# Kernel tuning notes

Measured on AMD Instinct MI355X. Metric: run time of the kernel, lower is better.

Reference implementation:

```python
import jax, jax.numpy as jnp
import numpy as np

B, N, M = 8, 1024, 1024
DIM2 = 1280          # config.dim * 2
KIN = 1344           # esm_dim + cell_line_dim
H, DK = 8, 64        # heads, attn_dim_key
SCALE = DK ** -0.5


def setup_inputs() -> dict:
    key = jax.random.key(0)
    ks = jax.random.split(key, 7)
    rna_reps = jax.random.normal(ks[0], (B, N, DIM2), dtype=jnp.float32)
    protein_reps = jax.random.normal(ks[1], (B, M, KIN), dtype=jnp.float32)
    # learned params (Linear stores weight [out, in])
    Wq = jax.random.normal(ks[2], (H * DK, DIM2), dtype=jnp.float32) * (DIM2 ** -0.5)
    bq = jnp.zeros((H * DK,), dtype=jnp.float32)
    Wk = jax.random.normal(ks[3], (H * DK, KIN), dtype=jnp.float32) * (KIN ** -0.5)
    bk = jnp.zeros((H * DK,), dtype=jnp.float32)
    rel_bias = jax.random.normal(ks[4], (1, H, 1, DK), dtype=jnp.float32)
    return {"rna_reps": rna_reps, "protein_reps": protein_reps,
            "Wq": Wq, "bq": bq, "Wk": Wk, "bk": bk, "rel_bias": rel_bias}


def reference(rna_reps, protein_reps, Wq, bq, Wk, bk, rel_bias):
    b = rna_reps.shape[0]
    q = rna_reps @ Wq.T + bq           # [b, n, h*dk]
    k = protein_reps @ Wk.T + bk       # [b, m, h*dk]
    q = q.reshape(b, N, H, DK).transpose(0, 2, 1, 3)   # b h n d
    k = k.reshape(b, M, H, DK).transpose(0, 2, 1, 3)   # b h m d
    q = q * SCALE
    logits = jnp.einsum('bhid,bhjd->bhij', q + rel_bias, k)  # [b,h,n,m]
    out = jnp.mean(logits, axis=1)     # mean over heads -> [b,n,m]
    # dropout p=0.0 (eval) -> identity
    return out
```

## Files before the change

### kernel.cpp

```cpp
#include <hip/hip_runtime.h>
#include <hip/hip_bf16.h>


typedef __bf16 bf16x8 __attribute__((ext_vector_type(8)));
typedef __bf16 bf16x4 __attribute__((ext_vector_type(4)));
typedef float f32x4 __attribute__((ext_vector_type(4)));

__device__ inline bf16x4 cvt4(const f32x4 a) {
    bf16x4 r;
    r[0] = (__bf16)a[0]; r[1] = (__bf16)a[1];
    r[2] = (__bf16)a[2]; r[3] = (__bf16)a[3];
    return r;
}

__global__ __launch_bounds__(256, 2)
void proj_all(const float* __restrict__ rna,  const float* __restrict__ prot,
              const float* __restrict__ Wq,   const float* __restrict__ bq,
              const float* __restrict__ Wk,   const float* __restrict__ bk,
              const float* __restrict__ rb,
              __bf16* __restrict__ qout, __bf16* __restrict__ kout)
{
    __shared__ __bf16 AS[2][128 * 64];
    __shared__ __bf16 WS[2][128 * 64];

    const int bid = blockIdx.x;
    const int wg  = (bid & 7) * 64 + (bid >> 3);
    const bool isQ = wg < 256;
    const int lwg  = isQ ? wg : wg - 256;
    const int brow = (lwg >> 2) * 128;
    const int bcol = (lwg & 3) * 128;

    const float* A    = isQ ? rna : prot;
    const float* W    = isQ ? Wq  : Wk;
    const float* bias = isQ ? bq  : bk;
    __bf16*      out  = isQ ? qout : kout;
    const int    K    = isQ ? 1280 : 1344;
    const int    nt   = K >> 6;

    const int tid  = threadIdx.x;
    const int lane = tid & 63;
    const int wid  = tid >> 6;
    const int wr   = wid >> 1;
    const int wc   = wid & 1;
    const int fr   = lane & 15;
    const int q4   = lane >> 4;

    const int rloc = wid * 32 + q4;
    const float* aGlob = A + (size_t)(brow + rloc) * K + fr * 4;
    const float* wGlob = W + (size_t)(bcol + rloc) * K + fr * 4;
    const int lb = rloc * 128 + (((fr >> 1) ^ (q4 << 1)) << 4) + (lane & 1) * 8;

    const int rmask = ((fr & 3) << 1) | ((fr >> 2) & 1);

    f32x4 acc[4][4] = {};
    f32x4 ra[8], rw[8];

    #pragma unroll
    for (int i = 0; i < 8; ++i) {
        ra[i] = *(const f32x4*)(aGlob + (size_t)(i * 4) * K);
        rw[i] = *(const f32x4*)(wGlob + (size_t)(i * 4) * K);
    }

    for (int t = 0; t < nt; ++t) {
        char* as = (char*)AS[t & 1];
        char* ws = (char*)WS[t & 1];
        __syncthreads();
        #pragma unroll
        for (int i = 0; i < 8; ++i) {
            *(bf16x4*)(as + ((lb ^ ((i & 1) << 4)) + i * 512)) = cvt4(ra[i]);
            *(bf16x4*)(ws + ((lb ^ ((i & 1) << 4)) + i * 512)) = cvt4(rw[i]);
        }
        if (t + 1 < nt) {
            const int k0n = (t + 1) * 64;
            #pragma unroll
            for (int i = 0; i < 8; ++i) {
                ra[i] = *(const f32x4*)(aGlob + (size_t)(i * 4) * K + k0n);
                rw[i] = *(const f32x4*)(wGlob + (size_t)(i * 4) * K + k0n);
            }
        }
        __builtin_amdgcn_sched_barrier(0);
        __syncthreads();

        #pragma unroll
        for (int kk = 0; kk < 2; ++kk) {
            bf16x8 af[4], bw[4];
            #pragma unroll
            for (int m = 0; m < 4; ++m)
                af[m] = *(const bf16x8*)(as + (wr * 64 + m * 16 + fr) * 128
                                            + (((kk * 4 + q4) ^ rmask) << 4));
            #pragma unroll
            for (int n = 0; n < 4; ++n)
                bw[n] = *(const bf16x8*)(ws + (wc * 64 + n * 16 + fr) * 128
                                            + (((kk * 4 + q4) ^ rmask) << 4));
            #pragma unroll
            for (int m = 0; m < 4; ++m)
                #pragma unroll
                for (int n = 0; n < 4; ++n)
                    acc[m][n] = __builtin_amdgcn_mfma_f32_16x16x32_bf16(af[m], bw[n], acc[m][n], 0, 0, 0);
        }
    }

    const int r0 = (lane >> 4) * 4;
    #pragma unroll
    for (int n = 0; n < 4; ++n) {
        const int c = bcol + wc * 64 + n * 16 + fr;
        const float bv = bias[c];
        const float rv = isQ ? rb[c] : 0.0f;
        #pragma unroll
        for (int m = 0; m < 4; ++m) {
            const int row = brow + wr * 64 + m * 16 + r0;
            #pragma unroll
            for (int j = 0; j < 4; ++j) {
                float v = acc[m][n][j] + bv;
                if (isQ) v = 0.125f * v + rv;
                out[(size_t)(row + j) * 512 + c] = (__bf16)v;
            }
        }
    }
}

__global__ __launch_bounds__(256, 2)
void attn_kernel(const __bf16* __restrict__ Q,
                 const __bf16* __restrict__ Kb,
                 float* __restrict__ out)
{
    __shared__ __bf16 As[128 * 64];
    __shared__ __bf16 Bs[128 * 64];

    const int tid  = threadIdx.x;
    const int lane = tid & 63;
    const int wid  = tid >> 6;
    const int wr   = wid >> 1;
    const int wc   = wid & 1;
    const int b    = blockIdx.z;
    const int brow = blockIdx.y * 128;
    const int bcol = blockIdx.x * 128;

    const __bf16* Qb = Q  + (size_t)b * 1024 * 512;
    const __bf16* Kp = Kb + (size_t)b * 1024 * 512;

    const int fr = lane & 15;
    const int q4 = lane >> 4;

    f32x4 acc[4][4] = {};

    const int lr3 = lane >> 3;
    const int m3  = ((lr3 & 3) << 1) | ((lr3 >> 2) & 1);
    const int scol = ((lane & 7) ^ m3) * 8;
    const int rmask = ((fr & 3) << 1) | ((fr >> 2) & 1);

    for (int k0 = 0; k0 < 512; k0 += 64) {
        __syncthreads();
        #pragma unroll
        for (int i = 0; i < 4; ++i) {
            const int rbase = wid * 32 + i * 8;
            const __bf16* sa = Qb + (size_t)(brow + rbase + lr3) * 512 + k0 + scol;
            const __bf16* sb = Kp + (size_t)(bcol + rbase + lr3) * 512 + k0 + scol;
            __builtin_amdgcn_global_load_lds(
                (const __attribute__((address_space(1))) void*)sa,
                (__attribute__((address_space(3))) void*)&As[rbase * 64], 16, 0, 0);
            __builtin_amdgcn_global_load_lds(
                (const __attribute__((address_space(1))) void*)sb,
                (__attribute__((address_space(3))) void*)&Bs[rbase * 64], 16, 0, 0);
        }
        __syncthreads();

        #pragma unroll
        for (int kk = 0; kk < 2; ++kk) {
            const int ci = kk * 4 + q4;
            bf16x8 af[4], bf_[4];
            #pragma unroll
            for (int m = 0; m < 4; ++m)
                af[m] = *(const bf16x8*)(&As[(wr * 64 + m * 16 + fr) * 64 + ((ci ^ rmask) << 3)]);
            #pragma unroll
            for (int n = 0; n < 4; ++n)
                bf_[n] = *(const bf16x8*)(&Bs[(wc * 64 + n * 16 + fr) * 64 + ((ci ^ rmask) << 3)]);
            #pragma unroll
            for (int m = 0; m < 4; ++m)
                #pragma unroll
                for (int n = 0; n < 4; ++n)
                    acc[m][n] = __builtin_amdgcn_mfma_f32_16x16x32_bf16(af[m], bf_[n], acc[m][n], 0, 0, 0);
        }
    }

    float* op = out + (size_t)b * 1024 * 1024;
    const int r0 = (lane >> 4) * 4;
    #pragma unroll
    for (int n = 0; n < 4; ++n) {
        const int col = bcol + wc * 64 + n * 16 + fr;
        #pragma unroll
        for (int m = 0; m < 4; ++m) {
            const int row = brow + wr * 64 + m * 16 + r0;
            #pragma unroll
            for (int j = 0; j < 4; ++j)
                op[(size_t)(row + j) * 1024 + col] = 0.125f * acc[m][n][j];
        }
    }
}

extern "C" void kernel_launch(void* const* d_in, const int* in_sizes, int n_in,
                              void* d_out, int out_size, void* d_ws, size_t ws_size,
                              hipStream_t stream) {
    const float* rna  = (const float*)d_in[0];
    const float* prot = (const float*)d_in[1];
    const float* Wq   = (const float*)d_in[2];
    const float* bq   = (const float*)d_in[3];
    const float* Wk   = (const float*)d_in[4];
    const float* bk   = (const float*)d_in[5];
    const float* rb   = (const float*)d_in[6];

    __bf16* qws = (__bf16*)d_ws;
    __bf16* kws = qws + (size_t)8192 * 512;

    proj_all<<<dim3(512), dim3(256), 0, stream>>>(rna, prot, Wq, bq, Wk, bk, rb, qws, kws);
    attn_kernel<<<dim3(8, 8, 8), dim3(256), 0, stream>>>(qws, kws, (float*)d_out);
}
```

Baseline: 62.08 us.

## Deepen projection prefetch pipeline with manual vmcnt waits and one barrier per step

Rewrites the projection GEMM main loop so activation tiles are prefetched two K-steps ahead into alternating register sets, while weight tiles stay one step ahead. Global loads are issued through inline asm, and each step waits with an explicit s_waitcnt vmcnt count instead of relying on compiler-inserted waits. Each K-step now uses a single workgroup barrier after staging into LDS, replacing the two __syncthreads. The aim is to keep more memory requests in flight on this bandwidth-bound fp32 input read and to cut synchronisation stalls. In exchange it raises register pressure and depends on hand-counted waitcnt values staying correct.

```diff
diff --git a/kernel.cpp b/kernel.cpp
--- a/kernel.cpp
+++ b/kernel.cpp
@@ -11,6 +11,11 @@
     r[0] = (__bf16)a[0]; r[1] = (__bf16)a[1];
     r[2] = (__bf16)a[2]; r[3] = (__bf16)a[3];
     return r;
+}
+
+__device__ inline void gload4(f32x4& dst, const float* p) {
+    asm volatile("global_load_dwordx4 %0, %1, off"
+                 : "=&v"(dst) : "v"(p) : "memory");
 }
 
 __global__ __launch_bounds__(256, 2)
@@ -49,56 +54,84 @@
     const float* aGlob = A + (size_t)(brow + rloc) * K + fr * 4;
     const float* wGlob = W + (size_t)(bcol + rloc) * K + fr * 4;
     const int lb = rloc * 128 + (((fr >> 1) ^ (q4 << 1)) << 4) + (lane & 1) * 8;
-
     const int rmask = ((fr & 3) << 1) | ((fr >> 2) & 1);
 
     f32x4 acc[4][4] = {};
-    f32x4 ra[8], rw[8];
-
-    #pragma unroll
-    for (int i = 0; i < 8; ++i) {
-        ra[i] = *(const f32x4*)(aGlob + (size_t)(i * 4) * K);
-        rw[i] = *(const f32x4*)(wGlob + (size_t)(i * 4) * K);
-    }
-
-    for (int t = 0; t < nt; ++t) {
-        char* as = (char*)AS[t & 1];
-        char* ws = (char*)WS[t & 1];
-        __syncthreads();
-        #pragma unroll
-        for (int i = 0; i < 8; ++i) {
-            *(bf16x4*)(as + ((lb ^ ((i & 1) << 4)) + i * 512)) = cvt4(ra[i]);
-            *(bf16x4*)(ws + ((lb ^ ((i & 1) << 4)) + i * 512)) = cvt4(rw[i]);
-        }
-        if (t + 1 < nt) {
-            const int k0n = (t + 1) * 64;
-            #pragma unroll
-            for (int i = 0; i < 8; ++i) {
-                ra[i] = *(const f32x4*)(aGlob + (size_t)(i * 4) * K + k0n);
-                rw[i] = *(const f32x4*)(wGlob + (size_t)(i * 4) * K + k0n);
-            }
-        }
-        __builtin_amdgcn_sched_barrier(0);
-        __syncthreads();
-
-        #pragma unroll
-        for (int kk = 0; kk < 2; ++kk) {
-            bf16x8 af[4], bw[4];
-            #pragma unroll
-            for (int m = 0; m < 4; ++m)
-                af[m] = *(const bf16x8*)(as + (wr * 64 + m * 16 + fr) * 128
-                                            + (((kk * 4 + q4) ^ rmask) << 4));
-            #pragma unroll
-            for (int n = 0; n < 4; ++n)
-                bw[n] = *(const bf16x8*)(ws + (wc * 64 + n * 16 + fr) * 128
-                                            + (((kk * 4 + q4) ^ rmask) << 4));
-            #pragma unroll
-            for (int m = 0; m < 4; ++m)
-                #pragma unroll
-                for (int n = 0; n < 4; ++n)
-                    acc[m][n] = __builtin_amdgcn_mfma_f32_16x16x32_bf16(af[m], bw[n], acc[m][n], 0, 0, 0);
-        }
-    }
+    f32x4 a0[8], a1[8], wv[8];
+
+#define ISSUE_A(k0, ra) do {                                              \
+    _Pragma("unroll")                                                     \
+    for (int i_ = 0; i_ < 8; ++i_)                                        \
+        gload4(ra[i_], aGlob + (size_t)(i_ * 4) * K + (k0));              \
+    } while (0)
+
+#define ISSUE_W(k0) do {                                                  \
+    _Pragma("unroll")                                                     \
+    for (int i_ = 0; i_ < 8; ++i_)                                        \
+        gload4(wv[i_], wGlob + (size_t)(i_ * 4) * K + (k0));              \
+    } while (0)
+
+#define STAGE(p, ra) do {                                                 \
+    char* as_ = (char*)AS[p]; char* ws_ = (char*)WS[p];                   \
+    _Pragma("unroll")                                                     \
+    for (int i_ = 0; i_ < 8; ++i_) {                                      \
+        *(bf16x4*)(as_ + ((lb ^ ((i_ & 1) << 4)) + i_ * 512)) = cvt4(ra[i_]); \
+        *(bf16x4*)(ws_ + ((lb ^ ((i_ & 1) << 4)) + i_ * 512)) = cvt4(wv[i_]); \
+    } } while (0)
+
+#define COMPUTE(p) do {                                                   \
+    const char* as_ = (const char*)AS[p];                                 \
+    const char* ws_ = (const char*)WS[p];                                 \
+    _Pragma("unroll")                                                     \
+    for (int kk_ = 0; kk_ < 2; ++kk_) {                                   \
+        bf16x8 af[4], bw[4];                                              \
+        _Pragma("unroll")                                                 \
+        for (int m_ = 0; m_ < 4; ++m_)                                    \
+            af[m_] = *(const bf16x8*)(as_ + (wr * 64 + m_ * 16 + fr) * 128 \
+                                          + (((kk_ * 4 + q4) ^ rmask) << 4)); \
+        _Pragma("unroll")                                                 \
+        for (int n_ = 0; n_ < 4; ++n_)                                    \
+            bw[n_] = *(const bf16x8*)(ws_ + (wc * 64 + n_ * 16 + fr) * 128 \
+                                          + (((kk_ * 4 + q4) ^ rmask) << 4)); \
+        _Pragma("unroll")                                                 \
+        for (int m_ = 0; m_ < 4; ++m_)                                    \
+            _Pragma("unroll")                                             \
+            for (int n_ = 0; n_ < 4; ++n_)                                \
+                acc[m_][n_] = __builtin_amdgcn_mfma_f32_16x16x32_bf16(    \
+                    af[m_], bw[n_], acc[m_][n_], 0, 0, 0);                \
+    } } while (0)
+
+#define STEP(t, p, ra) do {                                               \
+    if ((t) + 1 < nt) asm volatile("s_waitcnt vmcnt(8)" ::: "memory");    \
+    else              asm volatile("s_waitcnt vmcnt(0)" ::: "memory");    \
+    __builtin_amdgcn_sched_barrier(0);        \
+    STAGE(p, ra);                                                         \
+    __builtin_amdgcn_sched_barrier(0);                                    \
+    if ((t) + 1 < nt) ISSUE_W(((t) + 1) * 64);                            \
+    if ((t) + 2 < nt) ISSUE_A(((t) + 2) * 64, ra);                        \
+    __builtin_amdgcn_sched_barrier(0);                                    \
+    asm volatile("s_waitcnt lgkmcnt(0)" ::: "memory");    \
+    __builtin_amdgcn_s_barrier();          \
+    __builtin_amdgcn_sched_barrier(0);                                    \
+    COMPUTE(p);                                                           \
+} while (0)
+
+    ISSUE_A(0, a0);
+    ISSUE_W(0);
+    ISSUE_A(64, a1);
+
+    int t = 0;
+    for (; t + 1 < nt; t += 2) {
+        STEP(t,     0, a0);
+        STEP(t + 1, 1, a1);
+    }
+    if (t < nt) STEP(t, 0, a0);
+
+#undef ISSUE_A
+#undef ISSUE_W
+#undef STAGE
+#undef COMPUTE
+#undef STEP
 
     const int r0 = (lane >> 4) * 4;
     #pragma unroll
```

Result: faster. 60.19 us (-3.0%).

## Restructure projection GEMM into 256x128 tiles with a software-pipelined ping-pong LDS schedule

Applied to the files above, without the earlier changes.

The projection kernel now uses 512-thread blocks, each computing a 256x128 output tile, so the grid is 256 blocks instead of 512 and each weight tile is reused across twice as many rows. The main loop is rewritten as a two-stage software pipeline. Global loads are issued through inline asm two k-steps ahead, and explicit vmcnt waits split the fp32-to-bf16 LDS writes into two halves interleaved with the MFMA phases. Raw s_barrier and setprio are added around the MFMA bursts to overlap memory traffic with compute. The risks are the fragility of the hand-tuned waitcnt schedule and having only one block per CU to hide latency.

```diff
diff --git a/kernel.cpp b/kernel.cpp
--- a/kernel.cpp
+++ b/kernel.cpp
@@ -13,21 +13,31 @@
     return r;
 }
 
-__global__ __launch_bounds__(256, 2)
+__device__ inline void gload4(f32x4& dst, const float* p) {
+    asm volatile("global_load_dwordx4 %0, %1, off"
+                 : "=&v"(dst) : "v"(p) : "memory");
+}
+
+#define SCHB  __builtin_amdgcn_sched_barrier(0)
+#define BARR  __builtin_amdgcn_s_barrier()
+#define LGKM0 asm volatile("s_waitcnt lgkmcnt(0)" ::: "memory")
+#define WAITV(n_) asm volatile("s_waitcnt vmcnt(" #n_ ")" ::: "memory")
+
+__global__ __launch_bounds__(512, 2)
 void proj_all(const float* __restrict__ rna,  const float* __restrict__ prot,
               const float* __restrict__ Wq,   const float* __restrict__ bq,
               const float* __restrict__ Wk,   const float* __restrict__ bk,
               const float* __restrict__ rb,
               __bf16* __restrict__ qout, __bf16* __restrict__ kout)
 {
-    __shared__ __bf16 AS[2][128 * 64];
+    __shared__ __bf16 AS[2][256 * 64];
     __shared__ __bf16 WS[2][128 * 64];
 
     const int bid = blockIdx.x;
-    const int wg  = (bid & 7) * 64 + (bid >> 3);
-    const bool isQ = wg < 256;
-    const int lwg  = isQ ? wg : wg - 256;
-    const int brow = (lwg >> 2) * 128;
+    const int wg  = (bid & 7) * 32 + (bid >> 3);
+    const bool isQ = wg < 128;
+    const int lwg  = isQ ? wg : wg - 128;
+    const int brow = (lwg >> 2) * 256;
     const int bcol = (lwg & 3) * 128;
 
     const float* A    = isQ ? rna : prot;
@@ -45,60 +55,105 @@
     const int fr   = lane & 15;
     const int q4   = lane >> 4;
 
-    const int rloc = wid * 32 + q4;
-    const float* aGlob = A + (size_t)(brow + rloc) * K + fr * 4;
-    const float* wGlob = W + (size_t)(bcol + rloc) * K + fr * 4;
-    const int lb = rloc * 128 + (((fr >> 1) ^ (q4 << 1)) << 4) + (lane & 1) * 8;
-
+    const int rlocA = wid * 32 + q4;
+    const int rlocW = wid * 16 + q4;
+    const float* aGlob = A + (size_t)(brow + rlocA) * K + fr * 4;
+    const float* wGlob = W + (size_t)(bcol + rlocW) * K + fr * 4;
+    const int lbA = rlocA * 128 + (((fr >> 1) ^ (q4 << 1)) << 4) + (lane & 1) * 8;
+    const int lbW = rlocW * 128 + (((fr >> 1) ^ (q4 << 1)) << 4) + (lane & 1) * 8;
     const int rmask = ((fr & 3) << 1) | ((fr >> 2) & 1);
 
     f32x4 acc[4][4] = {};
-    f32x4 ra[8], rw[8];
-
-    #pragma unroll
-    for (int i = 0; i < 8; ++i) {
-        ra[i] = *(const f32x4*)(aGlob + (size_t)(i * 4) * K);
-        rw[i] = *(const f32x4*)(wGlob + (size_t)(i * 4) * K);
-    }
-
-    for (int t = 0; t < nt; ++t) {
-        char* as = (char*)AS[t & 1];
-        char* ws = (char*)WS[t & 1];
-        __syncthreads();
-        #pragma unroll
-        for (int i = 0; i < 8; ++i) {
-            *(bf16x4*)(as + ((lb ^ ((i & 1) << 4)) + i * 512)) = cvt4(ra[i]);
-            *(bf16x4*)(ws + ((lb ^ ((i & 1) << 4)) + i * 512)) = cvt4(rw[i]);
-        }
-        if (t + 1 < nt) {
-            const int k0n = (t + 1) * 64;
-            #pragma unroll
-            for (int i = 0; i < 8; ++i) {
-                ra[i] = *(const f32x4*)(aGlob + (size_t)(i * 4) * K + k0n);
-                rw[i] = *(const f32x4*)(wGlob + (size_t)(i * 4) * K + k0n);
-            }
-        }
-        __builtin_amdgcn_sched_barrier(0);
-        __syncthreads();
-
-        #pragma unroll
-        for (int kk = 0; kk < 2; ++kk) {
-            bf16x8 af[4], bw[4];
-            #pragma unroll
-            for (int m = 0; m < 4; ++m)
-                af[m] = *(const bf16x8*)(as + (wr * 64 + m * 16 + fr) * 128
-                                            + (((kk * 4 + q4) ^ rmask) << 4));
-            #pragma unroll
-            for (int n = 0; n < 4; ++n)
-                bw[n] = *(const bf16x8*)(ws + (wc * 64 + n * 16 + fr) * 128
-                                            + (((kk * 4 + q4) ^ rmask) << 4));
-            #pragma unroll
-            for (int m = 0; m < 4; ++m)
-                #pragma unroll
-                for (int n = 0; n < 4; ++n)
-                    acc[m][n] = __builtin_amdgcn_mfma_f32_16x16x32_bf16(af[m], bw[n], acc[m][n], 0, 0, 0);
-        }
-    }
+    f32x4 av[8], wv[4];
+
+#define ISS_A(i_, k0) gload4(av[i_], aGlob + (size_t)((i_) * 4) * K + (k0))
+#define ISS_W(j_, k0) gload4(wv[j_], wGlob + (size_t)((j_) * 4) * K + (k0))
+#define WR_A(i_, p_) *(bf16x4*)((char*)AS[p_] + ((lbA ^ (((i_) & 1) << 4)) + (i_) * 512)) = cvt4(av[i_])
+#define WR_W(j_, p_) *(bf16x4*)((char*)WS[p_] + ((lbW ^ (((j_) & 1) << 4)) + (j_) * 512)) = cvt4(wv[j_])
+#define RD_A(m_, kk_, p_) (*(const bf16x8*)((const char*)AS[p_] + (wr * 64 + (m_) * 16 + fr) * 128 + ((((kk_) * 4 + q4) ^ rmask) << 4)))
+#define RD_W(n_, kk_, p_) (*(const bf16x8*)((const char*)WS[p_] + (wc * 64 + (n_) * 16 + fr) * 128 + ((((kk_) * 4 + q4) ^ rmask) << 4)))
+#define MM(m_, n_, A_, B_) acc[m_][n_] = __builtin_amdgcn_mfma_f32_16x16x32_bf16(A_, B_, acc[m_][n_], 0, 0, 0)
+
+#define STEP(t, p) do {                                                    \
+    const int k2_ = ((t) + 2) * 64;                                        \
+    bf16x8 af0, af1, af2, af3, bw0, bw1, bw2, bw3;                         \
+                     \
+    if ((t) + 1 < nt) {                                                    \
+        WAITV(6);                                                          \
+        SCHB;                                                              \
+        WR_A(0, (p) ^ 1); WR_A(1, (p) ^ 1); WR_A(2, (p) ^ 1);              \
+        WR_A(3, (p) ^ 1); WR_A(4, (p) ^ 1); WR_A(5, (p) ^ 1);              \
+    }                                                                      \
+    if ((t) + 2 < nt) {                                                    \
+        ISS_A(0, k2_); ISS_A(1, k2_); ISS_A(2, k2_);                       \
+        ISS_A(3, k2_); ISS_A(4, k2_); ISS_A(5, k2_);                       \
+    }                                                                      \
+    af0 = RD_A(0, 0, p); af1 = RD_A(1, 0, p);                              \
+    af2 = RD_A(2, 0, p); af3 = RD_A(3, 0, p);                              \
+    bw0 = RD_W(0, 0, p); bw1 = RD_W(1, 0, p);                              \
+    bw2 = RD_W(2, 0, p); bw3 = RD_W(3, 0, p);                              \
+    BARR; LGKM0; SCHB;                                                     \
+    __builtin_amdgcn_s_setprio(1);                                         \
+    MM(0, 0, af0, bw0); MM(1, 0, af1, bw0); MM(2, 0, af2, bw0); MM(3, 0, af3, bw0); \
+    MM(0, 1, af0, bw1); MM(1, 1, af1, bw1); MM(2, 1, af2, bw1); MM(3, 1, af3, bw1); \
+    MM(0, 2, af0, bw2); MM(1, 2, af1, bw2); MM(2, 2, af2, bw2); MM(3, 2, af3, bw2); \
+    MM(0, 3, af0, bw3); MM(1, 3, af1, bw3); MM(2, 3, af2, bw3); MM(3, 3, af3, bw3); \
+    __builtin_amdgcn_s_setprio(0);                                         \
+    BARR;                                                                  \
+                     \
+    if ((t) + 1 < nt) {                                                    \
+        if ((t) + 2 < nt) { WAITV(6); } else { WAITV(0); }                 \
+        SCHB;                                                              \
+        WR_A(6, (p) ^ 1); WR_A(7, (p) ^ 1);                                \
+        WR_W(0, (p) ^ 1); WR_W(1, (p) ^ 1); WR_W(2, (p) ^ 1); WR_W(3, (p) ^ 1); \
+    }                                                                      \
+    if ((t) + 2 < nt) {                                                    \
+        ISS_A(6, k2_); ISS_A(7, k2_);                                      \
+        ISS_W(0, k2_); ISS_W(1, k2_); ISS_W(2, k2_); ISS_W(3, k2_);        \
+    }                                                                      \
+    af0 = RD_A(0, 1, p); af1 = RD_A(1, 1, p);                              \
+    af2 = RD_A(2, 1, p); af3 = RD_A(3, 1, p);                              \
+    bw0 = RD_W(0, 1, p); bw1 = RD_W(1, 1, p);                              \
+    bw2 = RD_W(2, 1, p); bw3 = RD_W(3, 1, p);                              \
+    BARR; LGKM0; SCHB;                                                     \
+    __builtin_amdgcn_s_setprio(1);                                         \
+    MM(0, 0, af0, bw0); MM(1, 0, af1, bw0); MM(2, 0, af2, bw0); MM(3, 0, af3, bw0); \
+    MM(0, 1, af0, bw1); MM(1, 1, af1, bw1); MM(2, 1, af2, bw1); MM(3, 1, af3, bw1); \
+    MM(0, 2, af0, bw2); MM(1, 2, af1, bw2); MM(2, 2, af2, bw2); MM(3, 2, af3, bw2); \
+    MM(0, 3, af0, bw3); MM(1, 3, af1, bw3); MM(2, 3, af2, bw3); MM(3, 3, af3, bw3); \
+    __builtin_amdgcn_s_setprio(0);                                         \
+    BARR;                                                                  \
+} while (0)
+
+    #pragma unroll
+    for (int i = 0; i < 8; ++i) ISS_A(i, 0);
+    #pragma unroll
+    for (int j = 0; j < 4; ++j) ISS_W(j, 0);
+    WAITV(0); SCHB;
+    #pragma unroll
+    for (int i = 0; i < 8; ++i) WR_A(i, 0);
+    #pragma unroll
+    for (int j = 0; j < 4; ++j) WR_W(j, 0);
+    #pragma unroll
+    for (int i = 0; i < 8; ++i) ISS_A(i, 64);
+    #pragma unroll
+    for (int j = 0; j < 4; ++j) ISS_W(j, 64);
+    SCHB; LGKM0; BARR; SCHB;
+
+    for (int t = 0; t + 1 < nt; t += 2) {
+        STEP(t, 0);
+        STEP(t + 1, 1);
+    }
+    if (nt & 1) STEP(nt - 1, 0);
+
+#undef ISS_A
+#undef ISS_W
+#undef WR_A
+#undef WR_W
+#undef RD_A
+#undef RD_W
+#undef MM
+#undef STEP
 
     const int r0 = (lane >> 4) * 4;
     #pragma unroll
@@ -212,6 +267,6 @@
     __bf16* qws = (__bf16*)d_ws;
     __bf16* kws = qws + (size_t)8192 * 512;
 
-    proj_all<<<dim3(512), dim3(256), 0, stream>>>(rna, prot, Wq, bq, Wk, bk, rb, qws, kws);
+    proj_all<<<dim3(256), dim3(512), 0, stream>>>(rna, prot, Wq, bq, Wk, bk, rb, qws, kws);
     attn_kernel<<<dim3(8, 8, 8), dim3(256), 0, stream>>>(qws, kws, (float*)d_out);
 }
```

Result: faster. 59.23 us (-4.6%).

## Pre-convert weights to bf16 and load MFMA operands directly from global memory

Applied to the files above, without the earlier changes.

Adds a small kernel that converts Wq and Wk to bf16 in workspace on every call. The projection kernel then drops its LDS staging: each wave loads its A rows (fp32) and W rows (bf16) straight into registers in MFMA fragment layout, using a two-deep register double buffer with explicit vmcnt waits and s_setprio around the MFMA bursts. This removes the LDS writes and reads and the block barriers, but each wave now loads its operands without sharing them through LDS, so global and L2 traffic rises and register pressure grows. It also adds one extra kernel launch.

```diff
diff --git a/kernel.cpp b/kernel.cpp
--- a/kernel.cpp
+++ b/kernel.cpp
@@ -13,16 +13,46 @@
     return r;
 }
 
+__device__ inline bf16x8 cvt2(const f32x4 a, const f32x4 b) {
+    bf16x8 r;
+    r[0] = (__bf16)a[0]; r[1] = (__bf16)a[1]; r[2] = (__bf16)a[2]; r[3] = (__bf16)a[3];
+    r[4] = (__bf16)b[0]; r[5] = (__bf16)b[1]; r[6] = (__bf16)b[2]; r[7] = (__bf16)b[3];
+    return r;
+}
+
+__device__ inline void gload4(f32x4& dst, const float* p) {
+    asm volatile("global_load_dwordx4 %0, %1, off"
+                 : "=&v"(dst) : "v"(p) : "memory");
+}
+__device__ inline void gload4b(bf16x8& dst, const __bf16* p) {
+    asm volatile("global_load_dwordx4 %0, %1, off"
+                 : "=&v"(dst) : "v"(p) : "memory");
+}
+
+#define SCHB  __builtin_amdgcn_sched_barrier(0)
+#define WAITV(n_) asm volatile("s_waitcnt vmcnt(" #n_ ")" ::: "memory")
+
+__global__ __launch_bounds__(256)
+void wcvt(const float* __restrict__ Wq, const float* __restrict__ Wk,
+          __bf16* __restrict__ wqb, __bf16* __restrict__ wkb)
+{
+    const int NQ = 512 * 1280 / 4;
+    const int s  = blockIdx.x * 256 + threadIdx.x;
+    if (s < NQ) {
+        ((bf16x4*)wqb)[s] = cvt4(((const f32x4*)Wq)[s]);
+    } else {
+        const int t = s - NQ;
+        ((bf16x4*)wkb)[t] = cvt4(((const f32x4*)Wk)[t]);
+    }
+}
+
 __global__ __launch_bounds__(256, 2)
 void proj_all(const float* __restrict__ rna,  const float* __restrict__ prot,
-              const float* __restrict__ Wq,   const float* __restrict__ bq,
-              const float* __restrict__ Wk,   const float* __restrict__ bk,
+              const __bf16* __restrict__ wqb, const __bf16* __restrict__ wkb,
+              const float* __restrict__ bq,   const float* __restrict__ bk,
               const float* __restrict__ rb,
               __bf16* __restrict__ qout, __bf16* __restrict__ kout)
 {
-    __shared__ __bf16 AS[2][128 * 64];
-    __shared__ __bf16 WS[2][128 * 64];
-
     const int bid = blockIdx.x;
     const int wg  = (bid & 7) * 64 + (bid >> 3);
     const bool isQ = wg < 256;
@@ -30,12 +60,12 @@
     const int brow = (lwg >> 2) * 128;
     const int bcol = (lwg & 3) * 128;
 
-    const float* A    = isQ ? rna : prot;
-    const float* W    = isQ ? Wq  : Wk;
-    const float* bias = isQ ? bq  : bk;
-    __bf16*      out  = isQ ? qout : kout;
-    const int    K    = isQ ? 1280 : 1344;
-    const int    nt   = K >> 6;
+    const float*  A    = isQ ? rna : prot;
+    const __bf16* Wb   = isQ ? wqb : wkb;
+    const float*  bias = isQ ? bq  : bk;
+    __bf16*       out  = isQ ? qout : kout;
+    const int     K    = isQ ? 1280 : 1344;
+    const int     U    = K >> 5;
 
     const int tid  = threadIdx.x;
     const int lane = tid & 63;
@@ -45,62 +75,58 @@
     const int fr   = lane & 15;
     const int q4   = lane >> 4;
 
-    const int rloc = wid * 32 + q4;
-    const float* aGlob = A + (size_t)(brow + rloc) * K + fr * 4;
-    const float* wGlob = W + (size_t)(bcol + rloc) * K + fr * 4;
-    const int lb = rloc * 128 + (((fr >> 1) ^ (q4 << 1)) << 4) + (lane & 1) * 8;
-
-    const int rmask = ((fr & 3) << 1) | ((fr >> 2) & 1);
-
-    f32x4 acc[4][4] = {};
-    f32x4 ra[8], rw[8];
-
-    #pragma unroll
-    for (int i = 0; i < 8; ++i) {
-        ra[i] = *(const f32x4*)(aGlob + (size_t)(i * 4) * K);
-        rw[i] = *(const f32x4*)(wGlob + (size_t)(i * 4) * K);
-    }
-
-    for (int t = 0; t < nt; ++t) {
-        char* as = (char*)AS[t & 1];
-        char* ws = (char*)WS[t & 1];
-        __syncthreads();
-        #pragma unroll
-        for (int i = 0; i < 8; ++i) {
-            *(bf16x4*)(as + ((lb ^ ((i & 1) << 4)) + i * 512)) = cvt4(ra[i]);
-            *(bf16x4*)(ws + ((lb ^ ((i & 1) << 4)) + i * 512)) = cvt4(rw[i]);
-        }
-        if (t + 1 < nt) {
-            const int k0n = (t + 1) * 64;
-            #pragma unroll
-            for (int i = 0; i < 8; ++i) {
-                ra[i] = *(const f32x4*)(aGlob + (size_t)(i * 4) * K + k0n);
-                rw[i] = *(const f32x4*)(wGlob + (size_t)(i * 4) * K + k0n);
-            }
-        }
-        __builtin_amdgcn_sched_barrier(0);
-        __syncthreads();
-
-        #pragma unroll
-        for (int kk = 0; kk < 2; ++kk) {
-            bf16x8 af[4], bw[4];
-            #pragma unroll
-            for (int m = 0; m < 4; ++m)
-                af[m] = *(const bf16x8*)(as + (wr * 64 + m * 16 + fr) * 128
-                                            + (((kk * 4 + q4) ^ rmask) << 4));
-            #pragma unroll
-            for (int n = 0; n < 4; ++n)
-                bw[n] = *(const bf16x8*)(ws + (wc * 64 + n * 16 + fr) * 128
-                                            + (((kk * 4 + q4) ^ rmask) << 4));
-            #pragma unroll
-            for (int m = 0; m < 4; ++m)
-                #pragma unroll
-                for (int n = 0; n < 4; ++n)
-                    acc[m][n] = __builtin_amdgcn_mfma_f32_16x16x32_bf16(af[m], bw[n], acc[m][n], 0, 0, 0);
-        }
-    }
-
-    const int r0 = (lane >> 4) * 4;
+    const float*  aB0 = A  + (size_t)(brow + wr * 64 +  0 + fr) * K + q4 * 8;
+    const float*  aB1 = A  + (size_t)(brow + wr * 64 + 16 + fr) * K + q4 * 8;
+    const float*  aB2 = A  + (size_t)(brow + wr * 64 + 32 + fr) * K + q4 * 8;
+    const float*  aB3 = A  + (size_t)(brow + wr * 64 + 48 + fr) * K + q4 * 8;
+    const __bf16* wB0 = Wb + (size_t)(bcol + wc * 64 +  0 + fr) * K + q4 * 8;
+    const __bf16* wB1 = Wb + (size_t)(bcol + wc * 64 + 16 + fr) * K + q4 * 8;
+    const __bf16* wB2 = Wb + (size_t)(bcol + wc * 64 + 32 + fr) * K + q4 * 8;
+    const __bf16* wB3 = Wb + (size_t)(bcol + wc * 64 + 48 + fr) * K + q4 * 8;
+
+    f32x4  acc[4][4] = {};
+    f32x4  sa0[8], sa1[8];
+    bf16x8 sw0[4], sw1[4];
+
+#define MM(m_, n_, A_, B_) acc[m_][n_] = __builtin_amdgcn_mfma_f32_16x16x32_bf16(A_, B_, acc[m_][n_], 0, 0, 0)
+
+#define ISSUE(u_, sa, sw) do {                                            \
+    const int ko_ = (u_) * 32;                                            \
+    gload4(sa[0], aB0 + ko_); gload4(sa[1], aB0 + ko_ + 4);               \
+    gload4(sa[2], aB1 + ko_); gload4(sa[3], aB1 + ko_ + 4);               \
+    gload4(sa[4], aB2 + ko_); gload4(sa[5], aB2 + ko_ + 4);               \
+    gload4(sa[6], aB3 + ko_); gload4(sa[7], aB3 + ko_ + 4);               \
+    gload4b(sw[0], wB0 + ko_); gload4b(sw[1], wB1 + ko_);                 \
+    gload4b(sw[2], wB2 + ko_); gload4b(sw[3], wB3 + ko_);                 \
+} while (0)
+
+#define PHASE(u_, sa, sw) do {                                            \
+    if ((u_) + 1 < U) { WAITV(12); } else { WAITV(0); }                   \
+    SCHB;                                                                 \
+    bf16x8 a0_ = cvt2(sa[0], sa[1]), a1_ = cvt2(sa[2], sa[3]);            \
+    bf16x8 a2_ = cvt2(sa[4], sa[5]), a3_ = cvt2(sa[6], sa[7]);            \
+    __builtin_amdgcn_s_setprio(1);                                        \
+    MM(0, 0, a0_, sw[0]); MM(1, 0, a1_, sw[0]); MM(2, 0, a2_, sw[0]); MM(3, 0, a3_, sw[0]); \
+    MM(0, 1, a0_, sw[1]); MM(1, 1, a1_, sw[1]); MM(2, 1, a2_, sw[1]); MM(3, 1, a3_, sw[1]); \
+    MM(0, 2, a0_, sw[2]); MM(1, 2, a1_, sw[2]); MM(2, 2, a2_, sw[2]); MM(3, 2, a3_, sw[2]); \
+    MM(0, 3, a0_, sw[3]); MM(1, 3, a1_, sw[3]); MM(2, 3, a2_, sw[3]); MM(3, 3, a3_, sw[3]); \
+    __builtin_amdgcn_s_setprio(0);                                        \
+    if ((u_) + 2 < U) ISSUE((u_) + 2, sa, sw);                            \
+} while (0)
+
+    ISSUE(0, sa0, sw0);
+    ISSUE(1, sa1, sw1);
+
+    for (int u = 0; u < U; u += 2) {
+        PHASE(u,     sa0, sw0);
+        PHASE(u + 1, sa1, sw1);
+    }
+
+#undef ISSUE
+#undef PHASE
+#undef MM
+
+    const int r0 = q4 * 4;
     #pragma unroll
     for (int n = 0; n < 4; ++n) {
         const int c = bcol + wc * 64 + n * 16 + fr;
@@ -211,7 +237,10 @@
 
     __bf16* qws = (__bf16*)d_ws;
     __bf16* kws = qws + (size_t)8192 * 512;
-
-    proj_all<<<dim3(512), dim3(256), 0, stream>>>(rna, prot, Wq, bq, Wk, bk, rb, qws, kws);
+    __bf16* wqb = kws + (size_t)8192 * 512;
+    __bf16* wkb = wqb + (size_t)512 * 1280;
+
+    wcvt<<<dim3(1312), dim3(256), 0, stream>>>(Wq, Wk, wqb, wkb);
+    proj_all<<<dim3(512), dim3(256), 0, stream>>>(rna, prot, wqb, wkb, bq, bk, rb, qws, kws);
     attn_kernel<<<dim3(8, 8, 8), dim3(256), 0, stream>>>(qws, kws, (float*)d_out);
 }
```

Result: slower. 140.7 us (+126.6%).
